# Optimization experiments

Hardware: AMD Instinct MI355X
Metric: run time of the kernel (lower is better)

Reference implementation:

```python
import jax, jax.numpy as jnp
import numpy as np

B, T = 16, 2048
V, E, H, C = 32000, 512, 4, 3  # vocab, embed, heads, context (history 2 + current)
EPS = 1e-5


def setup_inputs() -> dict:
    key = jax.random.key(0)
    k0, k1, k2, k3, k4, k5, k6 = jax.random.split(key, 7)
    tokens = jax.random.randint(k0, (B, T), 0, V)
    embed_table = jax.random.normal(k1, (V, E), dtype=jnp.float32)
    pos = jax.random.normal(k2, (H, E, C), dtype=jnp.float32) * (1.0 / np.sqrt(H))
    ffn_w = jax.random.normal(k3, (E, E), dtype=jnp.float32) * (1.0 / np.sqrt(E))
    ffn_b = jax.random.normal(k4, (E,), dtype=jnp.float32) * 0.01
    ln_g = jnp.ones((E,), dtype=jnp.float32)
    ln_b = jnp.zeros((E,), dtype=jnp.float32)
    return {"tokens": tokens, "embed_table": embed_table, "pos": pos,
            "ffn_w": ffn_w, "ffn_b": ffn_b, "ln_g": ln_g, "ln_b": ln_b}


def reference(tokens, embed_table, pos, ffn_w, ffn_b, ln_g, ln_b):
    # embed lookup: [B, T, E]
    x = embed_table[tokens]
    # prepend zero history, extract sliding windows of size C: [B, T, C, E]
    x_cat = jnp.concatenate([jnp.zeros((B, C - 1, E), dtype=x.dtype), x], axis=1)
    x_win = jnp.stack([x_cat[:, i:i + T] for i in range(C)], axis=2)
    # multi-head positional scores: pos viewed as [H, C, E]
    pos_hce = jnp.transpose(pos, (0, 2, 1))  # [H, C, E]
    w = jnp.einsum('btce,hce->bthc', x_win, pos_hce)          # scores
    out = jnp.einsum('bthc,btce->bte', w, x_win) / (H * C)    # weighted sum
    # FFN (torch Linear: y = x @ W^T + b)
    out = out @ ffn_w.T + ffn_b
    # LayerNorm
    mu = jnp.mean(out, axis=-1, keepdims=True)
    var = jnp.mean(jnp.square(out - mu), axis=-1, keepdims=True)
    out = (out - mu) * jax.lax.rsqrt(var + EPS) * ln_g + ln_b
    # swish
    return out * jax.nn.sigmoid(out)
```

## Files before the change

### kernel.cpp

```cpp
#include <hip/hip_runtime.h>
#include <hip/hip_bf16.h>


#define Bq 16
#define Tq 2048
#define Eq 512
#define Cq 3
#define Hq 4
#define Mq (Bq * Tq)
#define LN_EPS 1e-5f

typedef __attribute__((ext_vector_type(8))) short bf16x8;
typedef __attribute__((ext_vector_type(4))) float f32x4;

__device__ __forceinline__ unsigned short f2bf(float f) {
    unsigned int u = __float_as_uint(f);
    u += 0x7fffu + ((u >> 16) & 1u);
    return (unsigned short)(u >> 16);
}
__device__ __forceinline__ unsigned int cvt_pk_bf16(float lo, float hi) {
    unsigned int r;
    asm("v_cvt_pk_bf16_f32 %0, %1, %2" : "=v"(r) : "v"(lo), "v"(hi));
    return r;
}
__device__ __forceinline__ int xaddr(int row, int kbyte) {
    return row * 1024 + (kbyte ^ ((row & 7) << 4));
}

__global__ void prep_kernel(const float* __restrict__ pos,
                            const float* __restrict__ ffn_w,
                            float* __restrict__ Pt,
                            unsigned short* __restrict__ Wb) {
    int i = blockIdx.x * blockDim.x + threadIdx.x;
    if (i < Cq * Eq) {
        int c = i / Eq, e = i % Eq;
        float s = 0.f;
#pragma unroll
        for (int h = 0; h < Hq; ++h) s += pos[(h * Eq + e) * Cq + c];
        Pt[i] = s;
    }
    int nth = blockDim.x * gridDim.x;
    for (int j = i; j < Eq * Eq; j += nth) Wb[j] = f2bf(ffn_w[j]);
}

__global__ __launch_bounds__(512, 2) void fused_kernel(const int* __restrict__ tokens,
                                                       const float* __restrict__ tbl,
                                                       const float* __restrict__ Pt,
                                                       const unsigned short* __restrict__ Wb,
                                                       const float* __restrict__ bias,
                                                       const float* __restrict__ ln_g,
                                                       const float* __restrict__ ln_b,
                                                       float* __restrict__ out) {
    __shared__ __align__(16) unsigned short Atile[64 * 512];
    __shared__ float lds_sum[64][8];
    __shared__ float lds_sq[64][8];
    __shared__ float lds_mu[64];
    __shared__ float lds_rs[64];

    const int tid = threadIdx.x;
    const int wave = tid >> 6;
    const int lane = tid & 63;
    const int lr = lane & 15;
    const int lg = lane >> 4;
    const int m0 = blockIdx.x << 6;
    const int t0w = (m0 & (Tq - 1)) + (wave << 3);
    const int tb = (m0 >> 11) << 11;
    char* Xc = reinterpret_cast<char*>(Atile);

    const int n0 = wave << 6;
    const short* Bp = reinterpret_cast<const short*>(Wb) + (long)n0 * Eq;

    float x[10][8];
#pragma unroll
    for (int li = 0; li < 10; ++li) {
        const int t = t0w - 2 + li;
        float4 v0 = {0.f, 0.f, 0.f, 0.f}, v1 = {0.f, 0.f, 0.f, 0.f};
        if (t >= 0) {
            const int tok = tokens[tb + t];
            const float4* rp = reinterpret_cast<const float4*>(tbl + (long)tok * Eq + lane * 8);
            v0 = rp[0]; v1 = rp[1];
        }
        x[li][0] = v0.x; x[li][1] = v0.y; x[li][2] = v0.z; x[li][3] = v0.w;
        x[li][4] = v1.x; x[li][5] = v1.y; x[li][6] = v1.z; x[li][7] = v1.w;
    }

    bf16x8 br[2][8];
#pragma unroll
    for (int ks = 0; ks < 2; ++ks)
#pragma unroll
        for (int nf = 0; nf < 4; ++nf) {
            br[0][ks * 4 + nf] = *reinterpret_cast<const bf16x8*>(Bp + (nf * 16 + lr) * Eq + 0 * 64 + ks * 32 + lg * 8);
            br[1][ks * 4 + nf] = *reinterpret_cast<const bf16x8*>(Bp + (nf * 16 + lr) * Eq + 1 * 64 + ks * 32 + lg * 8);
        }

    float pv[Cq][8];
#pragma unroll
    for (int c = 0; c < Cq; ++c) {
        const float4* pp = reinterpret_cast<const float4*>(Pt + c * Eq + lane * 8);
        float4 p0 = pp[0], p1 = pp[1];
        pv[c][0] = p0.x; pv[c][1] = p0.y; pv[c][2] = p0.z; pv[c][3] = p0.w;
        pv[c][4] = p1.x; pv[c][5] = p1.y; pv[c][6] = p1.z; pv[c][7] = p1.w;
    }
    float d[10][Cq];
#pragma unroll
    for (int li = 0; li < 10; ++li)
#pragma unroll
        for (int c = 0; c < Cq; ++c)
            if (li >= c && li - c <= 7) {
                float s = 0.f;
#pragma unroll
                for (int e = 0; e < 8; ++e) s += x[li][e] * pv[c][e];
                d[li][c] = s;
            }
#pragma unroll
    for (int li = 0; li < 10; ++li)
#pragma unroll
        for (int c = 0; c < Cq; ++c)
            if (li >= c && li - c <= 7) {
#pragma unroll
                for (int m = 1; m < 64; m <<= 1) d[li][c] += __shfl_xor(d[li][c], m, 64);
            }

    const float inv = 1.f / (Hq * Cq);
#pragma unroll
    for (int jj = 0; jj < 8; ++jj) {
        const float s0 = d[jj][0] * inv, s1 = d[jj + 1][1] * inv, s2 = d[jj + 2][2] * inv;
        float a[8];
#pragma unroll
        for (int e = 0; e < 8; ++e)
            a[e] = s0 * x[jj][e] + s1 * x[jj + 1][e] + s2 * x[jj + 2][e];
        uint4 o;
        o.x = cvt_pk_bf16(a[0], a[1]);
        o.y = cvt_pk_bf16(a[2], a[3]);
        o.z = cvt_pk_bf16(a[4], a[5]);
        o.w = cvt_pk_bf16(a[6], a[7]);
        const int row = (wave << 3) + jj;
        *reinterpret_cast<uint4*>(Xc + xaddr(row, lane * 16)) = o;
    }
    __syncthreads();

    f32x4 acc[4][4];
#pragma unroll
    for (int i = 0; i < 4; ++i)
#pragma unroll
        for (int j = 0; j < 4; ++j) acc[i][j] = (f32x4){0.f, 0.f, 0.f, 0.f};

#pragma unroll
    for (int kb = 0; kb < 8; ++kb) {
#pragma unroll
        for (int ks = 0; ks < 2; ++ks) {
            bf16x8 af[4];
#pragma unroll
            for (int mf = 0; mf < 4; ++mf) {
                const int r = mf * 16 + lr;
                af[mf] = *reinterpret_cast<const bf16x8*>(Xc + xaddr(r, kb * 128 + ks * 64 + lg * 16));
            }
#pragma unroll
            for (int mf = 0; mf < 4; ++mf)
#pragma unroll
                for (int nf = 0; nf < 4; ++nf)
                    acc[mf][nf] = __builtin_amdgcn_mfma_f32_16x16x32_bf16(af[mf], br[kb & 1][ks * 4 + nf], acc[mf][nf], 0, 0, 0);
        }
        if (kb < 6) {
#pragma unroll
            for (int ks = 0; ks < 2; ++ks)
#pragma unroll
                for (int nf = 0; nf < 4; ++nf)
                    br[kb & 1][ks * 4 + nf] = *reinterpret_cast<const bf16x8*>(Bp + (nf * 16 + lr) * Eq + (kb + 2) * 64 + ks * 32 + lg * 8);
        }
    }

    float bcol[4];
#pragma unroll
    for (int nf = 0; nf < 4; ++nf) bcol[nf] = bias[n0 + nf * 16 + lr];

#pragma unroll
    for (int mf = 0; mf < 4; ++mf) {
#pragma unroll
        for (int i = 0; i < 4; ++i) {
            float sm = 0.f, sq = 0.f;
#pragma unroll
            for (int nf = 0; nf < 4; ++nf) {
                float v = acc[mf][nf][i] + bcol[nf];
                acc[mf][nf][i] = v;
                sm += v;
                sq += v * v;
            }
#pragma unroll
            for (int msk = 1; msk < 16; msk <<= 1) {
                sm += __shfl_xor(sm, msk, 64);
                sq += __shfl_xor(sq, msk, 64);
            }
            if (lr == 0) {
                const int row = mf * 16 + lg * 4 + i;
                lds_sum[row][wave] = sm;
                lds_sq[row][wave] = sq;
            }
        }
    }
    __syncthreads();
    if (tid < 64) {
        float sm = 0.f, sq = 0.f;
#pragma unroll
        for (int w = 0; w < 8; ++w) { sm += lds_sum[tid][w]; sq += lds_sq[tid][w]; }
        const float mu = sm * (1.f / Eq);
        const float var = sq * (1.f / Eq) - mu * mu;
        lds_mu[tid] = mu;
        lds_rs[tid] = rsqrtf(var + LN_EPS);
    }
    __syncthreads();

    float gcol[4], bbcol[4];
#pragma unroll
    for (int nf = 0; nf < 4; ++nf) {
        gcol[nf] = ln_g[n0 + nf * 16 + lr];
        bbcol[nf] = ln_b[n0 + nf * 16 + lr];
    }
#pragma unroll
    for (int mf = 0; mf < 4; ++mf) {
#pragma unroll
        for (int i = 0; i < 4; ++i) {
            const int row = mf * 16 + lg * 4 + i;
            const float mu = lds_mu[row];
            const float rs = lds_rs[row];
#pragma unroll
            for (int nf = 0; nf < 4; ++nf) {
                float v = acc[mf][nf][i];
                float o = (v - mu) * rs * gcol[nf] + bbcol[nf];
                o = o / (1.f + __expf(-o));
                out[(long)(m0 + row) * Eq + (n0 + nf * 16 + lr)] = o;
            }
        }
    }
}

extern "C" void kernel_launch(void* const* d_in, const int* in_sizes, int n_in,
                              void* d_out, int out_size, void* d_ws, size_t ws_size,
                              hipStream_t stream) {
    const int* tokens = (const int*)d_in[0];
    const float* tbl = (const float*)d_in[1];
    const float* pos = (const float*)d_in[2];
    const float* ffn_w = (const float*)d_in[3];
    const float* ffn_b = (const float*)d_in[4];
    const float* ln_g = (const float*)d_in[5];
    const float* ln_b = (const float*)d_in[6];
    float* out = (float*)d_out;

    char* ws = (char*)d_ws;
    float* Pt = (float*)ws;
    unsigned short* Wb = (unsigned short*)(ws + 8192);

    hipLaunchKernelGGL(prep_kernel, dim3(64), dim3(256), 0, stream, pos, ffn_w, Pt, Wb);
    hipLaunchKernelGGL(fused_kernel, dim3(Mq / 64), dim3(512), 0, stream,
                       tokens, tbl, Pt, Wb, ffn_b, ln_g, ln_b, out);
}
```

Baseline: 72.05 us.

## Shrink block to 32 rows with 4 waves covering 128 columns each

Block size drops from 64 rows and 8 waves to 32 rows and 4 waves. Each wave now computes a 32x128 output tile (2x8 MFMA fragments) instead of 64x64. The register double-buffered prefetch of W fragments is dropped; each k-step loads its B fragments directly before the MFMAs. Halving the LDS tile and using a 256-thread launch bound aims to double the number of resident blocks and the grid size, at the cost of more W reloads per output row and no prefetch overlap.

Result: slower. 101.7 us (+41.1%).

```diff
diff --git a/kernel.cpp b/kernel.cpp
--- a/kernel.cpp
+++ b/kernel.cpp
@@ -43,7 +43,7 @@
     for (int j = i; j < Eq * Eq; j += nth) Wb[j] = f2bf(ffn_w[j]);
 }
 
-__global__ __launch_bounds__(512, 2) void fused_kernel(const int* __restrict__ tokens,
+__global__ __launch_bounds__(256, 4) void fused_kernel(const int* __restrict__ tokens,
                                                        const float* __restrict__ tbl,
                                                        const float* __restrict__ Pt,
                                                        const unsigned short* __restrict__ Wb,
@@ -51,23 +51,23 @@
                                                        const float* __restrict__ ln_g,
                                                        const float* __restrict__ ln_b,
                                                        float* __restrict__ out) {
-    __shared__ __align__(16) unsigned short Atile[64 * 512];
-    __shared__ float lds_sum[64][8];
-    __shared__ float lds_sq[64][8];
-    __shared__ float lds_mu[64];
-    __shared__ float lds_rs[64];
+    __shared__ __align__(16) unsigned short Atile[32 * 512];
+    __shared__ float lds_sum[32][4];
+    __shared__ float lds_sq[32][4];
+    __shared__ float lds_mu[32];
+    __shared__ float lds_rs[32];
 
     const int tid = threadIdx.x;
     const int wave = tid >> 6;
     const int lane = tid & 63;
     const int lr = lane & 15;
     const int lg = lane >> 4;
-    const int m0 = blockIdx.x << 6;
+    const int m0 = blockIdx.x << 5;
     const int t0w = (m0 & (Tq - 1)) + (wave << 3);
     const int tb = (m0 >> 11) << 11;
     char* Xc = reinterpret_cast<char*>(Atile);
 
-    const int n0 = wave << 6;
+    const int n0 = wave << 7;
     const short* Bp = reinterpret_cast<const short*>(Wb) + (long)n0 * Eq;
 
     float x[10][8];
@@ -84,34 +84,19 @@
         x[li][4] = v1.x; x[li][5] = v1.y; x[li][6] = v1.z; x[li][7] = v1.w;
     }
 
-    bf16x8 br[2][8];
-#pragma unroll
-    for (int ks = 0; ks < 2; ++ks)
-#pragma unroll
-        for (int nf = 0; nf < 4; ++nf) {
-            br[0][ks * 4 + nf] = *reinterpret_cast<const bf16x8*>(Bp + (nf * 16 + lr) * Eq + 0 * 64 + ks * 32 + lg * 8);
-            br[1][ks * 4 + nf] = *reinterpret_cast<const bf16x8*>(Bp + (nf * 16 + lr) * Eq + 1 * 64 + ks * 32 + lg * 8);
-        }
-
-    float pv[Cq][8];
+    float d[10][Cq];
 #pragma unroll
     for (int c = 0; c < Cq; ++c) {
         const float4* pp = reinterpret_cast<const float4*>(Pt + c * Eq + lane * 8);
-        float4 p0 = pp[0], p1 = pp[1];
-        pv[c][0] = p0.x; pv[c][1] = p0.y; pv[c][2] = p0.z; pv[c][3] = p0.w;
-        pv[c][4] = p1.x; pv[c][5] = p1.y; pv[c][6] = p1.z; pv[c][7] = p1.w;
-    }
-    float d[10][Cq];
-#pragma unroll
-    for (int li = 0; li < 10; ++li)
-#pragma unroll
-        for (int c = 0; c < Cq; ++c)
+        const float4 p0 = pp[0], p1 = pp[1];
+#pragma unroll
+        for (int li = 0; li < 10; ++li) {
             if (li >= c && li - c <= 7) {
-                float s = 0.f;
-#pragma unroll
-                for (int e = 0; e < 8; ++e) s += x[li][e] * pv[c][e];
-                d[li][c] = s;
-            }
+                d[li][c] = x[li][0] * p0.x + x[li][1] * p0.y + x[li][2] * p0.z + x[li][3] * p0.w
+                         + x[li][4] * p1.x + x[li][5] * p1.y + x[li][6] * p1.z + x[li][7] * p1.w;
+            }
+        }
+    }
 #pragma unroll
     for (int li = 0; li < 10; ++li)
 #pragma unroll
@@ -139,48 +124,42 @@
     }
     __syncthreads();
 
-    f32x4 acc[4][4];
-#pragma unroll
-    for (int i = 0; i < 4; ++i)
-#pragma unroll
-        for (int j = 0; j < 4; ++j) acc[i][j] = (f32x4){0.f, 0.f, 0.f, 0.f};
+    f32x4 acc[2][8];
+#pragma unroll
+    for (int i = 0; i < 2; ++i)
+#pragma unroll
+        for (int j = 0; j < 8; ++j) acc[i][j] = (f32x4){0.f, 0.f, 0.f, 0.f};
 
 #pragma unroll
     for (int kb = 0; kb < 8; ++kb) {
 #pragma unroll
         for (int ks = 0; ks < 2; ++ks) {
-            bf16x8 af[4];
-#pragma unroll
-            for (int mf = 0; mf < 4; ++mf) {
-                const int r = mf * 16 + lr;
-                af[mf] = *reinterpret_cast<const bf16x8*>(Xc + xaddr(r, kb * 128 + ks * 64 + lg * 16));
-            }
-#pragma unroll
-            for (int mf = 0; mf < 4; ++mf)
-#pragma unroll
-                for (int nf = 0; nf < 4; ++nf)
-                    acc[mf][nf] = __builtin_amdgcn_mfma_f32_16x16x32_bf16(af[mf], br[kb & 1][ks * 4 + nf], acc[mf][nf], 0, 0, 0);
-        }
-        if (kb < 6) {
-#pragma unroll
-            for (int ks = 0; ks < 2; ++ks)
-#pragma unroll
-                for (int nf = 0; nf < 4; ++nf)
-                    br[kb & 1][ks * 4 + nf] = *reinterpret_cast<const bf16x8*>(Bp + (nf * 16 + lr) * Eq + (kb + 2) * 64 + ks * 32 + lg * 8);
-        }
-    }
-
-    float bcol[4];
-#pragma unroll
-    for (int nf = 0; nf < 4; ++nf) bcol[nf] = bias[n0 + nf * 16 + lr];
-
-#pragma unroll
-    for (int mf = 0; mf < 4; ++mf) {
+            bf16x8 af[2], bfv[8];
+#pragma unroll
+            for (int nf = 0; nf < 8; ++nf)
+                bfv[nf] = *reinterpret_cast<const bf16x8*>(Bp + (nf * 16 + lr) * Eq + kb * 64 + ks * 32 + lg * 8);
+#pragma unroll
+            for (int mf = 0; mf < 2; ++mf)
+                af[mf] = *reinterpret_cast<const bf16x8*>(Xc + xaddr(mf * 16 + lr, kb * 128 + ks * 64 + lg * 16));
+#pragma unroll
+            for (int mf = 0; mf < 2; ++mf)
+#pragma unroll
+                for (int nf = 0; nf < 8; ++nf)
+                    acc[mf][nf] = __builtin_amdgcn_mfma_f32_16x16x32_bf16(af[mf], bfv[nf], acc[mf][nf], 0, 0, 0);
+        }
+    }
+
+    float bcol[8];
+#pragma unroll
+    for (int nf = 0; nf < 8; ++nf) bcol[nf] = bias[n0 + nf * 16 + lr];
+
+#pragma unroll
+    for (int mf = 0; mf < 2; ++mf) {
 #pragma unroll
         for (int i = 0; i < 4; ++i) {
             float sm = 0.f, sq = 0.f;
 #pragma unroll
-            for (int nf = 0; nf < 4; ++nf) {
+            for (int nf = 0; nf < 8; ++nf) {
                 float v = acc[mf][nf][i] + bcol[nf];
                 acc[mf][nf][i] = v;
                 sm += v;
@@ -199,10 +178,10 @@
         }
     }
     __syncthreads();
-    if (tid < 64) {
+    if (tid < 32) {
         float sm = 0.f, sq = 0.f;
 #pragma unroll
-        for (int w = 0; w < 8; ++w) { sm += lds_sum[tid][w]; sq += lds_sq[tid][w]; }
+        for (int w = 0; w < 4; ++w) { sm += lds_sum[tid][w]; sq += lds_sq[tid][w]; }
         const float mu = sm * (1.f / Eq);
         const float var = sq * (1.f / Eq) - mu * mu;
         lds_mu[tid] = mu;
@@ -210,21 +189,21 @@
     }
     __syncthreads();
 
-    float gcol[4], bbcol[4];
-#pragma unroll
-    for (int nf = 0; nf < 4; ++nf) {
+    float gcol[8], bbcol[8];
+#pragma unroll
+    for (int nf = 0; nf < 8; ++nf) {
         gcol[nf] = ln_g[n0 + nf * 16 + lr];
         bbcol[nf] = ln_b[n0 + nf * 16 + lr];
     }
 #pragma unroll
-    for (int mf = 0; mf < 4; ++mf) {
+    for (int mf = 0; mf < 2; ++mf) {
 #pragma unroll
         for (int i = 0; i < 4; ++i) {
             const int row = mf * 16 + lg * 4 + i;
             const float mu = lds_mu[row];
             const float rs = lds_rs[row];
 #pragma unroll
-            for (int nf = 0; nf < 4; ++nf) {
+            for (int nf = 0; nf < 8; ++nf) {
                 float v = acc[mf][nf][i];
                 float o = (v - mu) * rs * gcol[nf] + bbcol[nf];
                 o = o / (1.f + __expf(-o));
@@ -251,6 +230,6 @@
     unsigned short* Wb = (unsigned short*)(ws + 8192);
 
     hipLaunchKernelGGL(prep_kernel, dim3(64), dim3(256), 0, stream, pos, ffn_w, Pt, Wb);
-    hipLaunchKernelGGL(fused_kernel, dim3(Mq / 64), dim3(512), 0, stream,
+    hipLaunchKernelGGL(fused_kernel, dim3(Mq / 32), dim3(256), 0, stream,
                        tokens, tbl, Pt, Wb, ffn_b, ln_g, ln_b, out);
 }
```
